# Performance work log

Measured on AMD Instinct MI355X. Metric: run time of the kernel, lower is better.

The kernel has to match this reference:

```python
import jax, jax.numpy as jnp
import numpy as np

NUM_NODES = 100000
NUM_EDGES = 2500000
NUM_GRAPHS = 512
NODE_DIM = 7
STATE_DIM = 32
M = 2
ROUNDS = 4


def setup_inputs() -> dict:
    key = jax.random.key(0)
    ks = jax.random.split(key, 16)
    x = jax.random.normal(ks[0], (NUM_NODES, NODE_DIM), dtype=jnp.float32)
    edge_index = jax.random.randint(ks[1], (2, NUM_EDGES), 0, NUM_NODES)
    batch = jnp.sort(jax.random.randint(ks[2], (NUM_NODES,), 0, NUM_GRAPHS))
    s = 1.0 / np.sqrt(STATE_DIM)
    W_in = jax.random.normal(ks[3], (NODE_DIM, STATE_DIM), dtype=jnp.float32) / np.sqrt(NODE_DIM)
    b_in = jnp.zeros((STATE_DIM,), dtype=jnp.float32)
    W_msg = jax.random.normal(ks[4], (ROUNDS, STATE_DIM, STATE_DIM), dtype=jnp.float32) * s
    b_msg = jnp.zeros((ROUNDS, STATE_DIM), dtype=jnp.float32)
    W_upd = jax.random.normal(ks[5], (ROUNDS, STATE_DIM, STATE_DIM), dtype=jnp.float32) * s
    b_upd = jnp.zeros((ROUNDS, STATE_DIM), dtype=jnp.float32)
    W_out = jax.random.normal(ks[6], (STATE_DIM, 2 * M), dtype=jnp.float32) * s
    b_out = jnp.zeros((2 * M,), dtype=jnp.float32)
    return {"x": x, "edge_index": edge_index, "batch": batch,
            "W_in": W_in, "b_in": b_in, "W_msg": W_msg, "b_msg": b_msg,
            "W_upd": W_upd, "b_upd": b_upd, "W_out": W_out, "b_out": b_out}


def reference(x, edge_index, batch, W_in, b_in, W_msg, b_msg, W_upd, b_upd, W_out, b_out):
    # input net
    state = jax.nn.relu(x @ W_in + b_in)  # (N, S)
    src, dst = edge_index[0], edge_index[1]
    for r in range(ROUNDS):
        message = jax.nn.relu(state @ W_msg[r] + b_msg[r])          # (N, S)
        gathered = message[src]                                      # (E, S) irregular gather
        aggregated = jax.ops.segment_sum(gathered, dst, num_segments=NUM_NODES)  # scatter-add
        state = state + jax.nn.relu(aggregated @ W_upd[r] + b_upd[r])
    graph_state = jax.ops.segment_sum(state, batch, num_segments=NUM_GRAPHS)     # (G, S)
    out = graph_state @ W_out + b_out                                # (G, 2M)
    mean, log_std = jnp.split(out, 2, axis=-1)
    # Gaussian head: return mean and std (scale = exp(log_std)) concatenated
    return jnp.concatenate([mean, jnp.exp(log_std)], axis=-1)
```

## Files before the change

kernel.cpp:

```cpp
#include <hip/hip_runtime.h>
#include <hip/hip_fp8.h>
#include <math.h>

#define N_NODES 100000
#define N_EDGES 2500000
#define N_GRAPHS 512
#define NODE_DIM 7
#define S 32
#define ROUNDS 4

#define BKT_SHIFT 8
#define BKT_NODES 256
#define NBKT ((N_NODES + BKT_NODES - 1) / BKT_NODES)
#define CAP 7168
#define NSLOT 64
#define SLOT_PAD 32

#define GN (N_NODES * S / 256)
#define GG (N_NODES / 16)

__device__ __forceinline__ void block_max_publish(float v, float* slots, int bid, int tid) {
    __shared__ float wmax[4];
#pragma unroll
    for (int o = 32; o > 0; o >>= 1) v = fmaxf(v, __shfl_xor(v, o, 64));
    if ((tid & 63) == 0) wmax[tid >> 6] = v;
    __syncthreads();
    if (tid == 0) {
        float m = fmaxf(fmaxf(wmax[0], wmax[1]), fmaxf(wmax[2], wmax[3]));
        atomicMax((unsigned int*)&slots[(bid & (NSLOT - 1)) * SLOT_PAD], __float_as_uint(m));
    }
}

__device__ __forceinline__ void acc4_fp8(unsigned int u, float& a0, float& a1,
                                         float& a2, float& a3) {
#if __has_builtin(__builtin_amdgcn_cvt_pk_f32_fp8)
    typedef float v2f __attribute__((ext_vector_type(2)));
    v2f lo = __builtin_amdgcn_cvt_pk_f32_fp8((int)u, false);
    v2f hi = __builtin_amdgcn_cvt_pk_f32_fp8((int)u, true);
    a0 += lo.x; a1 += lo.y; a2 += hi.x; a3 += hi.y;
#else
    __hip_fp8_e4m3 t0, t1, t2, t3;
    t0.__x = u & 0xff; t1.__x = (u >> 8) & 0xff;
    t2.__x = (u >> 16) & 0xff; t3.__x = (u >> 24) & 0xff;
    a0 += (float)t0; a1 += (float)t1; a2 += (float)t2; a3 += (float)t3;
#endif
}

__global__ void k_input(const float* __restrict__ x, const float* __restrict__ W_in,
                        const float* __restrict__ b_in, float* __restrict__ state,
                        float* __restrict__ graph_state, int* __restrict__ cursor,
                        float* __restrict__ tmpmax) {
    __shared__ float sW[NODE_DIM * S];
    __shared__ float sb[S];
    __shared__ float wmax[4];
    int tid = threadIdx.x;
    if (tid < NODE_DIM * S) sW[tid] = W_in[tid];
    if (tid < S) sb[tid] = b_in[tid];
    __syncthreads();
    int gid = blockIdx.x * blockDim.x + tid;
    if (gid < N_GRAPHS * S) graph_state[gid] = 0.f;
    if (gid < NBKT) cursor[gid] = 0;
    int n = gid >> 5, j = gid & 31;
    float acc = sb[j];
#pragma unroll
    for (int k = 0; k < NODE_DIM; k++) acc += x[n * NODE_DIM + k] * sW[k * S + j];
    float v = fmaxf(acc, 0.f);
    state[gid] = v;
#pragma unroll
    for (int o = 32; o > 0; o >>= 1) v = fmaxf(v, __shfl_xor(v, o, 64));
    if ((tid & 63) == 0) wmax[tid >> 6] = v;
    __syncthreads();
    if (tid == 0)
        tmpmax[blockIdx.x] = fmaxf(fmaxf(wmax[0], wmax[1]), fmaxf(wmax[2], wmax[3]));
}

__global__ void k_bin(const int* __restrict__ src, const int* __restrict__ dst,
                      int* __restrict__ cursor, int* __restrict__ binned,
                      const float* __restrict__ tmpmax, float* __restrict__ smax0) {
    __shared__ int cnt[NBKT];
    __shared__ int base[NBKT];
    __shared__ float red[16];
    int tid = threadIdx.x;
    if (blockIdx.x == 0) {
        float m = 0.f;
        for (int i = tid; i < GN; i += 1024) m = fmaxf(m, tmpmax[i]);
#pragma unroll
        for (int o = 32; o > 0; o >>= 1) m = fmaxf(m, __shfl_xor(m, o, 64));
        if ((tid & 63) == 0) red[tid >> 6] = m;
        __syncthreads();
        if (tid == 0) {
            float g = 0.f;
#pragma unroll
            for (int k = 0; k < 16; k++) g = fmaxf(g, red[k]);
            smax0[0] = g;
        } else if (tid < NSLOT) {
            smax0[tid * SLOT_PAD] = 0.f;
        }
    }
    int tile = (N_EDGES + gridDim.x - 1) / gridDim.x;
    int b0 = blockIdx.x * tile;
    int b1 = min(b0 + tile, N_EDGES);
    for (int i = tid; i < NBKT; i += blockDim.x) cnt[i] = 0;
    __syncthreads();
    for (int e = b0 + tid; e < b1; e += blockDim.x)
        atomicAdd(&cnt[dst[e] >> BKT_SHIFT], 1);
    __syncthreads();
    for (int i = tid; i < NBKT; i += blockDim.x) {
        int c = cnt[i];
        base[i] = c ? atomicAdd(&cursor[i], c) : 0;
        cnt[i] = 0;
    }
    __syncthreads();
    for (int e = b0 + tid; e < b1; e += blockDim.x) {
        int d = dst[e];
        int k = d >> BKT_SHIFT;
        int lpos = base[k] + atomicAdd(&cnt[k], 1);
        if (lpos < CAP)
            binned[(size_t)k * CAP + lpos] = (src[e] << BKT_SHIFT) | (d & (BKT_NODES - 1));
    }
}

__global__ void k_fill2(const int* __restrict__ cursor, int* __restrict__ binned,
                        int* __restrict__ row_beg, int* __restrict__ row_end) {
    __shared__ int stage[CAP];
    __shared__ int cnt[BKT_NODES];
    __shared__ int sm[BKT_NODES];
    int tid = threadIdx.x;
    int bkt = blockIdx.x;
    int beg = bkt * CAP;
    int m = min(cursor[bkt], CAP);
    for (int i = tid; i < m; i += 256) stage[i] = binned[beg + i];
    cnt[tid] = 0;
    __syncthreads();
    for (int i = tid; i < m; i += 256) atomicAdd(&cnt[stage[i] & (BKT_NODES - 1)], 1);
    __syncthreads();
    int v = cnt[tid];
    sm[tid] = v;
    __syncthreads();
    for (int off = 1; off < BKT_NODES; off <<= 1) {
        int add = (tid >= off) ? sm[tid - off] : 0;
        __syncthreads();
        sm[tid] += add;
        __syncthreads();
    }
    {
        int excl = sm[tid] - v;
        cnt[tid] = excl;
        int n = bkt * BKT_NODES + tid;
        if (n < N_NODES) { row_beg[n] = beg + excl; row_end[n] = beg + excl + v; }
    }
    __syncthreads();
    for (int i = tid; i < m; i += 256) {
        int ent = stage[i];
        int p = atomicAdd(&cnt[ent & (BKT_NODES - 1)], 1);
        binned[beg + p] = ent >> BKT_SHIFT;
    }
}

__global__ void k_msg(const float* __restrict__ state, const float* __restrict__ W,
                      const float* __restrict__ b, const float* __restrict__ smax_slots,
                      float* __restrict__ smax_next, float* __restrict__ inv_scale_out,
                      __hip_fp8_e4m3* __restrict__ message) {
    __shared__ float sW[S * S];
    __shared__ float sb[S];
    __shared__ float ssc[S];
    int tid = threadIdx.x;
    if (blockIdx.x < NSLOT && tid == 0) smax_next[blockIdx.x * SLOT_PAD] = 0.f;
    for (int i = tid; i < S * S; i += 256) sW[i] = W[i];
    if (tid < S) sb[tid] = b[tid];
    __syncthreads();
    if (tid < S) {
        float smax = 0.f;
#pragma unroll
        for (int k = 0; k < NSLOT; k++) smax = fmaxf(smax, smax_slots[k * SLOT_PAD]);
        float cs = 0.f;
#pragma unroll
        for (int k = 0; k < S; k++) cs += fabsf(sW[k * S + tid]);
        float bound = smax * cs + fabsf(sb[tid]) + 1e-20f;
        int e = (int)floorf(log2f(400.f / bound));
        e = max(-60, min(60, e));
        ssc[tid] = exp2f((float)e);
        if (blockIdx.x == 0) inv_scale_out[tid] = exp2f((float)-e);
    }
    __syncthreads();
    int gid = blockIdx.x * 256 + tid;
    int j = tid & 31;
    float my = state[gid];
    float acc = sb[j];
#pragma unroll
    for (int k = 0; k < S; k++) acc += __shfl(my, k, 32) * sW[k * S + j];
    float m = fminf(fmaxf(acc, 0.f) * ssc[j], 440.f);
    message[gid] = __hip_fp8_e4m3(m);
}

__global__ void k_gather_upd(const int* __restrict__ row_beg, const int* __restrict__ row_end,
                             const int* __restrict__ csr_src,
                             const unsigned char* __restrict__ message,
                             const float* __restrict__ W, const float* __restrict__ b,
                             const float* __restrict__ inv_scale,
                             float* __restrict__ state, float* __restrict__ smax_next) {
    __shared__ float sW[S * S];
    __shared__ float sb[S];
    __shared__ float si[S];
    int tid = threadIdx.x;
    for (int i = tid; i < S * S; i += 256) sW[i] = W[i];
    if (tid < S) { sb[tid] = b[tid]; si[tid] = inv_scale[tid]; }
    __syncthreads();
    int g = tid >> 5, j = tid & 31;
    int n0 = blockIdx.x * 16 + g * 2;
    int n1 = n0 + 1;
    int es = j >> 3;
    int qd = j & 7;
    int b0 = row_beg[n0], e0 = row_end[n0];
    int b1 = row_beg[n1], e1 = row_end[n1];
    float a0 = 0.f, a1 = 0.f, a2 = 0.f, a3 = 0.f;
    float c0 = 0.f, c1 = 0.f, c2 = 0.f, c3 = 0.f;
    for (; b0 < e0 || b1 < e1; b0 += 32, b1 += 32) {
        int sid0 = (b0 + j < e0) ? csr_src[b0 + j] : 0;
        int sid1 = (b1 + j < e1) ? csr_src[b1 + j] : 0;
        unsigned int u0[8], u1[8];
#pragma unroll
        for (int p = 0; p < 8; p++) {
            int s = __shfl(sid0, p * 4 + es, 32);
            unsigned int* ap = (unsigned int*)(message + (unsigned)s * 32u + (unsigned)qd * 4u);
            u0[p] = __hip_atomic_load(ap, __ATOMIC_RELAXED, __HIP_MEMORY_SCOPE_AGENT);
        }
#pragma unroll
        for (int p = 0; p < 8; p++) {
            int s = __shfl(sid1, p * 4 + es, 32);
            unsigned int* ap = (unsigned int*)(message + (unsigned)s * 32u + (unsigned)qd * 4u);
            u1[p] = __hip_atomic_load(ap, __ATOMIC_RELAXED, __HIP_MEMORY_SCOPE_AGENT);
        }
#pragma unroll
        for (int p = 0; p < 8; p++) {
            unsigned int uv = (b0 + p * 4 + es < e0) ? u0[p] : 0u;
            acc4_fp8(uv, a0, a1, a2, a3);
        }
#pragma unroll
        for (int p = 0; p < 8; p++) {
            unsigned int uv = (b1 + p * 4 + es < e1) ? u1[p] : 0u;
            acc4_fp8(uv, c0, c1, c2, c3);
        }
    }
    a0 += __shfl_xor(a0, 8, 32); a0 += __shfl_xor(a0, 16, 32);
    a1 += __shfl_xor(a1, 8, 32); a1 += __shfl_xor(a1, 16, 32);
    a2 += __shfl_xor(a2, 8, 32); a2 += __shfl_xor(a2, 16, 32);
    a3 += __shfl_xor(a3, 8, 32); a3 += __shfl_xor(a3, 16, 32);
    c0 += __shfl_xor(c0, 8, 32); c0 += __shfl_xor(c0, 16, 32);
    c1 += __shfl_xor(c1, 8, 32); c1 += __shfl_xor(c1, 16, 32);
    c2 += __shfl_xor(c2, 8, 32); c2 += __shfl_xor(c2, 16, 32);
    c3 += __shfl_xor(c3, 8, 32); c3 += __shfl_xor(c3, 16, 32);
    float s0 = si[4 * qd + 0], s1 = si[4 * qd + 1];
    float s2 = si[4 * qd + 2], s3 = si[4 * qd + 3];
    a0 *= s0; a1 *= s1; a2 *= s2; a3 *= s3;
    c0 *= s0; c1 *= s1; c2 *= s2; c3 *= s3;
    float u0v = sb[j], u1v = sb[j];
#pragma unroll
    for (int k = 0; k < S; k++) {
        float av, cv;
        switch (k & 3) {
            case 0: av = __shfl(a0, k >> 2, 32); cv = __shfl(c0, k >> 2, 32); break;
            case 1: av = __shfl(a1, k >> 2, 32); cv = __shfl(c1, k >> 2, 32); break;
            case 2: av = __shfl(a2, k >> 2, 32); cv = __shfl(c2, k >> 2, 32); break;
            default: av = __shfl(a3, k >> 2, 32); cv = __shfl(c3, k >> 2, 32); break;
        }
        float w = sW[k * S + j];
        u0v += av * w;
        u1v += cv * w;
    }
    size_t i0 = (size_t)n0 * S + j, i1 = (size_t)n1 * S + j;
    float ns0 = state[i0] + fmaxf(u0v, 0.f);
    float ns1 = state[i1] + fmaxf(u1v, 0.f);
    state[i0] = ns0;
    state[i1] = ns1;
    block_max_publish(fmaxf(ns0, ns1), smax_next, blockIdx.x, tid);
}

__global__ void k_pool(const float* __restrict__ state, const int* __restrict__ batch,
                       float* __restrict__ graph_state) {
    const int CHUNK = 32;
    const int nchunks = (N_NODES + CHUNK - 1) / CHUNK;
    int gid = blockIdx.x * blockDim.x + threadIdx.x;
    if (gid >= nchunks * S) return;
    int c = gid >> 5, j = gid & 31;
    int n0 = c * CHUNK;
    int n1 = min(n0 + CHUNK, N_NODES);
    float acc = 0.f;
    int curb = batch[n0];
    for (int n = n0; n < n1; n++) {
        int bn = batch[n];
        if (bn != curb) {
            atomicAdd(&graph_state[curb * S + j], acc);
            acc = 0.f;
            curb = bn;
        }
        acc += state[(size_t)n * S + j];
    }
    atomicAdd(&graph_state[curb * S + j], acc);
}

__global__ void k_head(const float* __restrict__ graph_state, const float* __restrict__ W_out,
                       const float* __restrict__ b_out, float* __restrict__ out) {
    int gid = blockIdx.x * blockDim.x + threadIdx.x;
    if (gid >= N_GRAPHS * 4) return;
    int g = gid >> 2, j = gid & 3;
    float acc = b_out[j];
#pragma unroll
    for (int k = 0; k < S; k++) acc += graph_state[g * S + k] * W_out[k * 4 + j];
    out[gid] = (j < 2) ? acc : expf(fminf(acc, 88.0f));
}

extern "C" void kernel_launch(void* const* d_in, const int* in_sizes, int n_in,
                              void* d_out, int out_size, void* d_ws, size_t ws_size,
                              hipStream_t stream) {
    const float* x     = (const float*)d_in[0];
    const int*   ei    = (const int*)d_in[1];
    const int*   batch = (const int*)d_in[2];
    const float* W_in  = (const float*)d_in[3];
    const float* b_in  = (const float*)d_in[4];
    const float* W_msg = (const float*)d_in[5];
    const float* b_msg = (const float*)d_in[6];
    const float* W_upd = (const float*)d_in[7];
    const float* b_upd = (const float*)d_in[8];
    const float* W_out = (const float*)d_in[9];
    const float* b_out = (const float*)d_in[10];
    float* out = (float*)d_out;

    float* state            = (float*)d_ws;
    __hip_fp8_e4m3* message = (__hip_fp8_e4m3*)(state + (size_t)N_NODES * S);
    float* graph_state      = (float*)((char*)message + (size_t)N_NODES * S);
    float* smax             = graph_state + N_GRAPHS * S;
    float* inv_scale        = smax + (ROUNDS + 1) * NSLOT * SLOT_PAD;
    float* tmpmax           = inv_scale + S;
    int*   row_beg          = (int*)(tmpmax + GN);
    int*   row_end          = row_beg + N_NODES;
    int*   cursor           = row_end + N_NODES;
    int*   binned           = cursor + NBKT;

    const int* src = ei;
    const int* dst = ei + N_EDGES;

    k_input<<<GN, dim3(256), 0, stream>>>(x, W_in, b_in, state, graph_state, cursor, tmpmax);
    k_bin<<<512, dim3(1024), 0, stream>>>(src, dst, cursor, binned, tmpmax, smax);
    k_fill2<<<NBKT, dim3(256), 0, stream>>>(cursor, binned, row_beg, row_end);

    for (int r = 0; r < ROUNDS; r++) {
        k_msg<<<GN, dim3(256), 0, stream>>>(state, W_msg + r * S * S, b_msg + r * S,
                                            smax + r * NSLOT * SLOT_PAD,
                                            smax + (r + 1) * NSLOT * SLOT_PAD,
                                            inv_scale, message);
        k_gather_upd<<<GG, dim3(256), 0, stream>>>(row_beg, row_end, binned,
                                                   (const unsigned char*)message,
                                                   W_upd + r * S * S, b_upd + r * S,
                                                   inv_scale, state,
                                                   smax + (r + 1) * NSLOT * SLOT_PAD);
    }

    const int CHUNK = 32;
    int nchunks = (N_NODES + CHUNK - 1) / CHUNK;
    int gP = (nchunks * S + 255) / 256;
    k_pool<<<gP, dim3(256), 0, stream>>>(state, batch, graph_state);

    k_head<<<(N_GRAPHS * 4 + 255) / 256, dim3(256), 0, stream>>>(graph_state, W_out, b_out, out);
}
```

Baseline: 372.4 us.

## Sort edges by bucket in LDS before writing binned output in k_bin

The binning kernel now stages each block's edge tile (packed values and bucket ids) in shared memory and counting-sorts it by bucket with a block-wide prefix scan. Each bucket's run is then written to the global binned array contiguously, replacing the scattered per-edge writes and the second read of src/dst. Global bucket cursors are padded to separate cache lines to reduce atomic contention, and the block size drops from 1024 to 512 threads. The large LDS footprint (about 24 KB per block) may limit occupancy, and the extra scan and sort passes add synchronisation.

```diff
diff --git a/kernel.cpp b/kernel.cpp
--- a/kernel.cpp
+++ b/kernel.cpp
@@ -15,6 +15,11 @@
 #define CAP 7168
 #define NSLOT 64
 #define SLOT_PAD 32
+#define CUR_PAD 32
+
+#define NBIN_BLOCKS 512
+#define NBIN_THREADS 512
+#define TILE ((N_EDGES + NBIN_BLOCKS - 1) / NBIN_BLOCKS)
 
 #define GN (N_NODES * S / 256)
 #define GG (N_NODES / 16)
@@ -59,7 +64,7 @@
     __syncthreads();
     int gid = blockIdx.x * blockDim.x + tid;
     if (gid < N_GRAPHS * S) graph_state[gid] = 0.f;
-    if (gid < NBKT) cursor[gid] = 0;
+    if (gid < NBKT * CUR_PAD) cursor[gid] = 0;
     int n = gid >> 5, j = gid & 31;
     float acc = sb[j];
 #pragma unroll
@@ -77,46 +82,72 @@
 __global__ void k_bin(const int* __restrict__ src, const int* __restrict__ dst,
                       int* __restrict__ cursor, int* __restrict__ binned,
                       const float* __restrict__ tmpmax, float* __restrict__ smax0) {
+    __shared__ int pval[TILE];
+    __shared__ unsigned short bkt[TILE];
+    __shared__ unsigned short sidx[TILE];
     __shared__ int cnt[NBKT];
     __shared__ int base[NBKT];
-    __shared__ float red[16];
+    __shared__ int gbase[NBKT];
+    __shared__ int sm[NBIN_THREADS];
+    __shared__ float red[8];
     int tid = threadIdx.x;
     if (blockIdx.x == 0) {
-        float m = 0.f;
-        for (int i = tid; i < GN; i += 1024) m = fmaxf(m, tmpmax[i]);
-#pragma unroll
-        for (int o = 32; o > 0; o >>= 1) m = fmaxf(m, __shfl_xor(m, o, 64));
-        if ((tid & 63) == 0) red[tid >> 6] = m;
+        float mx = 0.f;
+        for (int i = tid; i < GN; i += NBIN_THREADS) mx = fmaxf(mx, tmpmax[i]);
+#pragma unroll
+        for (int o = 32; o > 0; o >>= 1) mx = fmaxf(mx, __shfl_xor(mx, o, 64));
+        if ((tid & 63) == 0) red[tid >> 6] = mx;
         __syncthreads();
         if (tid == 0) {
             float g = 0.f;
 #pragma unroll
-            for (int k = 0; k < 16; k++) g = fmaxf(g, red[k]);
+            for (int k = 0; k < 8; k++) g = fmaxf(g, red[k]);
             smax0[0] = g;
         } else if (tid < NSLOT) {
             smax0[tid * SLOT_PAD] = 0.f;
         }
     }
-    int tile = (N_EDGES + gridDim.x - 1) / gridDim.x;
-    int b0 = blockIdx.x * tile;
-    int b1 = min(b0 + tile, N_EDGES);
-    for (int i = tid; i < NBKT; i += blockDim.x) cnt[i] = 0;
-    __syncthreads();
-    for (int e = b0 + tid; e < b1; e += blockDim.x)
-        atomicAdd(&cnt[dst[e] >> BKT_SHIFT], 1);
-    __syncthreads();
-    for (int i = tid; i < NBKT; i += blockDim.x) {
-        int c = cnt[i];
-        base[i] = c ? atomicAdd(&cursor[i], c) : 0;
-        cnt[i] = 0;
-    }
-    __syncthreads();
-    for (int e = b0 + tid; e < b1; e += blockDim.x) {
-        int d = dst[e];
+    int b0 = blockIdx.x * TILE;
+    int m = min(TILE, N_EDGES - b0);
+    if (m < 0) m = 0;
+    for (int k = tid; k < NBKT; k += NBIN_THREADS) cnt[k] = 0;
+    __syncthreads();
+    for (int i = tid; i < m; i += NBIN_THREADS) {
+        int d = dst[b0 + i];
+        int s = src[b0 + i];
         int k = d >> BKT_SHIFT;
-        int lpos = base[k] + atomicAdd(&cnt[k], 1);
+        pval[i] = (s << BKT_SHIFT) | (d & (BKT_NODES - 1));
+        bkt[i] = (unsigned short)k;
+        atomicAdd(&cnt[k], 1);
+    }
+    __syncthreads();
+    int v = (tid < NBKT) ? cnt[tid] : 0;
+    sm[tid] = v;
+    __syncthreads();
+    for (int off = 1; off < NBIN_THREADS; off <<= 1) {
+        int add = (tid >= off) ? sm[tid - off] : 0;
+        __syncthreads();
+        sm[tid] += add;
+        __syncthreads();
+    }
+    if (tid < NBKT) {
+        base[tid] = sm[tid] - v;
+        gbase[tid] = v ? atomicAdd(&cursor[tid * CUR_PAD], v) : 0;
+        cnt[tid] = 0;
+    }
+    __syncthreads();
+    for (int i = tid; i < m; i += NBIN_THREADS) {
+        int k = bkt[i];
+        int r = atomicAdd(&cnt[k], 1);
+        sidx[base[k] + r] = (unsigned short)i;
+    }
+    __syncthreads();
+    for (int i = tid; i < m; i += NBIN_THREADS) {
+        int e = sidx[i];
+        int k = bkt[e];
+        int lpos = gbase[k] + (i - base[k]);
         if (lpos < CAP)
-            binned[(size_t)k * CAP + lpos] = (src[e] << BKT_SHIFT) | (d & (BKT_NODES - 1));
+            binned[(size_t)k * CAP + lpos] = pval[e];
     }
 }
 
@@ -128,7 +159,7 @@
     int tid = threadIdx.x;
     int bkt = blockIdx.x;
     int beg = bkt * CAP;
-    int m = min(cursor[bkt], CAP);
+    int m = min(cursor[bkt * CUR_PAD], CAP);
     for (int i = tid; i < m; i += 256) stage[i] = binned[beg + i];
     cnt[tid] = 0;
     __syncthreads();
@@ -335,13 +366,13 @@
     int*   row_beg          = (int*)(tmpmax + GN);
     int*   row_end          = row_beg + N_NODES;
     int*   cursor           = row_end + N_NODES;
-    int*   binned           = cursor + NBKT;
+    int*   binned           = cursor + NBKT * CUR_PAD;
 
     const int* src = ei;
     const int* dst = ei + N_EDGES;
 
     k_input<<<GN, dim3(256), 0, stream>>>(x, W_in, b_in, state, graph_state, cursor, tmpmax);
-    k_bin<<<512, dim3(1024), 0, stream>>>(src, dst, cursor, binned, tmpmax, smax);
+    k_bin<<<NBIN_BLOCKS, dim3(NBIN_THREADS), 0, stream>>>(src, dst, cursor, binned, tmpmax, smax);
     k_fill2<<<NBKT, dim3(256), 0, stream>>>(cursor, binned, row_beg, row_end);
 
     for (int r = 0; r < ROUNDS; r++) {
```

Result: faster. 363.0 us (-2.5%).
